# Performance work log

Measured on AMD Instinct MI355X. Metric: run time of the kernel, lower is better.

The kernel has to match this reference:

```python
import jax, jax.numpy as jnp
import numpy as np

NNZ = 4_194_304
IN_FEATURES = 4096
OUT_FEATURES = 4096
BATCH = 4
SEQ = 2048


def setup_inputs() -> dict:
    key = jax.random.key(0)
    k1, k2, k3, k4, k5, k6 = jax.random.split(key, 6)
    x = jax.random.normal(k1, (BATCH, SEQ, IN_FEATURES), dtype=jnp.float32)
    rows = jax.random.randint(k2, (NNZ,), 0, OUT_FEATURES, dtype=jnp.int32)
    cols = jax.random.randint(k3, (NNZ,), 0, IN_FEATURES, dtype=jnp.int32)
    w_real = jax.random.normal(k4, (NNZ,), dtype=jnp.float32)
    w_imag = jax.random.normal(k5, (NNZ,), dtype=jnp.float32)
    phase_angles = jax.random.uniform(k6, (BATCH,), dtype=jnp.float32) * 2.0 * np.pi
    return {
        "x": x,
        "rows": rows,
        "cols": cols,
        "w_real": w_real,
        "w_imag": w_imag,
        "phase_angles": phase_angles,
        "out_features": OUT_FEATURES,
    }


def reference(x, rows, cols, w_real, w_imag, phase_angles, out_features):
    B, S, F_in = x.shape
    N = B * S
    x_flat = x.reshape(N, F_in)  # [N, F_in]
    # per-flattened-row cosine phase (phase is per-batch, repeated over seq)
    cos_p = jnp.cos(jnp.repeat(phase_angles, S))  # [N]
    # assemble sparse COO weights into dense (out, in) matrices (duplicates sum)
    Wr = jnp.zeros((out_features, F_in), dtype=x_flat.dtype).at[rows, cols].add(w_real)
    Wi = jnp.zeros((out_features, F_in), dtype=x_flat.dtype).at[rows, cols].add(w_imag)
    # out[n, r] = sum_e x[n, cols[e]] * (w_real[e] + cos(phase[n]) * w_imag[e])
    out = x_flat @ Wr.T + cos_p[:, None] * (x_flat @ Wi.T)  # [N, out]
    return out.reshape(B, S, out_features)
```

## Files before the change

kernel.cpp:

```cpp
#include <hip/hip_runtime.h>


#define K_IN   4096
#define F_OUT  4096
#define SEQ    2048
#define NROW   8192
#define NNZ    4194304
#define WELEM  16777216
#define NBUCK  1024
#define SEGB   5120

typedef float  f32x4  __attribute__((ext_vector_type(4)));
typedef __bf16 bf16x8 __attribute__((ext_vector_type(8)));
typedef unsigned short u16x8 __attribute__((ext_vector_type(8)));

__device__ __forceinline__ unsigned short f2bf(float f) {
  unsigned u = __builtin_bit_cast(unsigned, f);
  u += 0x7fffu + ((u >> 16) & 1u);
  return (unsigned short)(u >> 16);
}
__device__ __forceinline__ float bf2f(unsigned short b) {
  return __builtin_bit_cast(float, (unsigned)b << 16);
}

__global__ __launch_bounds__(1024) void bin_kernel(
    const int* __restrict__ rows, const int* __restrict__ cols,
    const float* __restrict__ wre, const float* __restrict__ wim,
    unsigned* __restrict__ cursor, unsigned long long* __restrict__ records,
    const float* __restrict__ x, unsigned short* __restrict__ Xb) {
  const int b = blockIdx.x;
  if (b < 256) {
    __shared__ unsigned cnt[NBUCK];
    const int tid = threadIdx.x;
    const int e0 = b << 14;
    cnt[tid] = 0u;
    __syncthreads();
    #pragma unroll
    for (int i = 0; i < 16; ++i)
      atomicAdd(&cnt[((unsigned)rows[e0 + (i << 10) + tid]) >> 2], 1u);
    __syncthreads();
    {
      const unsigned c = cnt[tid];
      unsigned base = 0u;
      if (c) base = atomicAdd(&cursor[tid], c);
      cnt[tid] = base;
    }
    __syncthreads();
    for (int i = 0; i < 16; ++i) {
      const int e = e0 + (i << 10) + tid;
      const unsigned r  = (unsigned)rows[e];
      const unsigned bk = r >> 2;
      const unsigned rank = atomicAdd(&cnt[bk], 1u);
      const unsigned pk = (unsigned)f2bf(wre[e]) | ((unsigned)f2bf(wim[e]) << 16);
      if (rank < SEGB)
        records[(size_t)bk * SEGB + rank] =
            ((unsigned long long)pk << 32) | ((r & 3u) << 12) | (unsigned)cols[e];
    }
  } else {
    const size_t i8 = (((size_t)(b - 256) << 10) + threadIdx.x) << 3;
    f32x4 a = *(const f32x4*)(x + i8);
    f32x4 c = *(const f32x4*)(x + i8 + 4);
    u16x8 v;
    v[0] = f2bf(a[0]); v[1] = f2bf(a[1]); v[2] = f2bf(a[2]); v[3] = f2bf(a[3]);
    v[4] = f2bf(c[0]); v[5] = f2bf(c[1]); v[6] = f2bf(c[2]); v[7] = f2bf(c[3]);
    *(u16x8*)(Xb + i8) = v;
  }
}

__global__ __launch_bounds__(1024) void assemble_kernel(
    const unsigned* __restrict__ cursor,
    const unsigned long long* __restrict__ records,
    const float* __restrict__ phase, unsigned short* __restrict__ Wb) {
  __shared__ float accRe[16384];
  __shared__ float accIm[16384];
  const int bk  = blockIdx.x;
  const int tid = threadIdx.x;
  #pragma unroll
  for (int i = 0; i < 16; ++i) {
    accRe[(i << 10) + tid] = 0.f;
    accIm[(i << 10) + tid] = 0.f;
  }
  __syncthreads();
  unsigned cnt = cursor[bk];
  if (cnt > SEGB) cnt = SEGB;
  const unsigned long long* seg = records + (size_t)bk * SEGB;
  for (unsigned i = tid; i < cnt; i += 1024) {
    const unsigned long long rec = seg[i];
    const unsigned s = (unsigned)rec & 16383u;
    atomicAdd(&accRe[s], bf2f((unsigned short)((rec >> 32) & 0xffffu)));
    atomicAdd(&accIm[s], bf2f((unsigned short)(rec >> 48)));
  }
  __syncthreads();
  float cb[4];
  cb[0] = cosf(phase[0]); cb[1] = cosf(phase[1]);
  cb[2] = cosf(phase[2]); cb[3] = cosf(phase[3]);
  #pragma unroll
  for (int it = 0; it < 16; ++it) {
    const int s = (it << 10) + tid;
    const float re = accRe[s];
    const float im = accIm[s];
    #pragma unroll
    for (int bb = 0; bb < 4; ++bb)
      Wb[((size_t)bb << 24) + ((size_t)bk << 14) + s] = f2bf(re + cb[bb] * im);
  }
}

#define GLOAD_LDS(g, l)                                                        \
  __builtin_amdgcn_global_load_lds(                                            \
      (const __attribute__((address_space(1))) unsigned int*)(g),              \
      (__attribute__((address_space(3))) unsigned int*)(l), 16, 0, 0)

__global__ __launch_bounds__(512, 2) void gemm_kernel(
    const unsigned short* __restrict__ Xb,
    const unsigned short* __restrict__ Wb,
    float* __restrict__ out) {
  __shared__ unsigned short lds[65536];

  const int tid  = threadIdx.x;
  const int wid  = tid >> 6;
  const int lane = tid & 63;
  const int wr   = wid >> 2;
  const int wc   = wid & 3;

  const int bid  = blockIdx.x;
  const int swz  = ((bid & 7) << 6) | (bid >> 3);
  const int brow = swz >> 4;
  const int bcol = swz & 15;
  const size_t M0 = (size_t)brow << 8;
  const int batch = brow >> 3;
  const unsigned short* Ap = Xb + M0 * K_IN;
  const unsigned short* Bp = Wb + ((size_t)batch << 24) + (((size_t)bcol << 8) * K_IN);

  const int srow = lane >> 3;
  const int gsl  = ((lane & 7) ^ srow) << 3;
  const int lrow = lane & 15;
  const int lr7  = lane & 7;
  const int sb   = lane >> 4;

  f32x4 acc[8][4] = {};

#define STAGE(buf, k0)                                                         \
  {                                                                            \
    _Pragma("unroll")                                                          \
    for (int l = 0; l < 4; ++l) {                                              \
      const int rr = (l << 6) + (wid << 3);                                    \
      GLOAD_LDS(Ap + (size_t)(rr + srow) * K_IN + (size_t)((k0) + gsl),        \
                &lds[((buf) << 15) + (rr << 6)]);                              \
    }                                                                          \
    _Pragma("unroll")                                                          \
    for (int l = 0; l < 4; ++l) {                                              \
      const int rr = (l << 6) + (wid << 3);                                    \
      GLOAD_LDS(Bp + (size_t)(rr + srow) * K_IN + (size_t)((k0) + gsl),        \
                &lds[((buf) << 15) + 16384 + (rr << 6)]);                      \
    }                                                                          \
  }

#define COMPUTE(buf)                                                           \
  {                                                                            \
    const unsigned short* la = &lds[(buf) << 15];                              \
    const unsigned short* lb = &lds[((buf) << 15) + 16384];                    \
    _Pragma("unroll")                                                          \
    for (int t = 0; t < 2; ++t) {                                              \
      const int cs = (((t << 2) + sb) ^ lr7) << 3;                             \
      bf16x8 af[8], bff[4];                                                    \
      _Pragma("unroll")                                                        \
      for (int m = 0; m < 8; ++m)                                              \
        af[m] = *(const bf16x8*)&la[(((wr << 7) + (m << 4) + lrow) << 6) + cs];\
      _Pragma("unroll")                                                        \
      for (int n = 0; n < 4; ++n)                                              \
        bff[n] = *(const bf16x8*)&lb[(((wc << 6) + (n << 4) + lrow) << 6) + cs];\
      __builtin_amdgcn_s_setprio(1);                                           \
      _Pragma("unroll")                                                        \
      for (int m = 0; m < 8; ++m)                                              \
        _Pragma("unroll")                                                      \
        for (int n = 0; n < 4; ++n)                                            \
          acc[m][n] = __builtin_amdgcn_mfma_f32_16x16x32_bf16(                 \
              af[m], bff[n], acc[m][n], 0, 0, 0);                              \
      __builtin_amdgcn_s_setprio(0);                                           \
    }                                                                          \
  }

  STAGE(0, 0);
  int cur = 0;
  for (int t = 0; t < 63; ++t) {
    STAGE(cur ^ 1, (t + 1) << 6);
    asm volatile("s_waitcnt vmcnt(8)\n\ts_barrier" ::: "memory");
    COMPUTE(cur);
    asm volatile("s_waitcnt lgkmcnt(0)\n\ts_barrier" ::: "memory");
    cur ^= 1;
  }
  asm volatile("s_waitcnt vmcnt(0)\n\ts_barrier" ::: "memory");
  COMPUTE(cur);

  const int ch = lane >> 4;
  float* op = out + (M0 + (size_t)(wr << 7)) * F_OUT + ((size_t)bcol << 8) + (wc << 6);
  #pragma unroll
  for (int m = 0; m < 8; ++m)
    #pragma unroll
    for (int n = 0; n < 4; ++n)
      #pragma unroll
      for (int j = 0; j < 4; ++j)
        op[(size_t)((m << 4) + (ch << 2) + j) * F_OUT + (n << 4) + lrow] = acc[m][n][j];
#undef STAGE
#undef COMPUTE
}

__global__ __launch_bounds__(256) void scatter_kernel(
    const int* __restrict__ rows, const int* __restrict__ cols,
    const float* __restrict__ wre, const float* __restrict__ wim,
    unsigned short* __restrict__ Wcb) {
  int e = blockIdx.x * 256 + threadIdx.x;
  int r = rows[e];
  int c = cols[e];
  unsigned pk = (unsigned)f2bf(wre[e]) | ((unsigned)f2bf(wim[e]) << 16);
  size_t idx = ((size_t)r << 12) + (size_t)c;
  asm volatile("global_atomic_pk_add_bf16 %0, %1, off"
               :: "v"(Wcb + (idx << 1)), "v"(pk) : "memory");
}
__global__ __launch_bounds__(256) void fold_kernel(
    const unsigned short* __restrict__ Wcb, const float* __restrict__ phase,
    unsigned short* __restrict__ Wb) {
  size_t i8 = ((size_t)blockIdx.x * 256 + threadIdx.x) << 3;
  float cb[4];
  cb[0] = cosf(phase[0]); cb[1] = cosf(phase[1]);
  cb[2] = cosf(phase[2]); cb[3] = cosf(phase[3]);
  const unsigned short* p = Wcb + (i8 << 1);
  u16x8 a = *(const u16x8*)(p);
  u16x8 b = *(const u16x8*)(p + 8);
  float rr[8], ii[8];
  rr[0] = bf2f(a[0]); ii[0] = bf2f(a[1]);
  rr[1] = bf2f(a[2]); ii[1] = bf2f(a[3]);
  rr[2] = bf2f(a[4]); ii[2] = bf2f(a[5]);
  rr[3] = bf2f(a[6]); ii[3] = bf2f(a[7]);
  rr[4] = bf2f(b[0]); ii[4] = bf2f(b[1]);
  rr[5] = bf2f(b[2]); ii[5] = bf2f(b[3]);
  rr[6] = bf2f(b[4]); ii[6] = bf2f(b[5]);
  rr[7] = bf2f(b[6]); ii[7] = bf2f(b[7]);
  #pragma unroll
  for (int bb = 0; bb < 4; ++bb) {
    float c = cb[bb];
    u16x8 v;
    #pragma unroll
    for (int j = 0; j < 8; ++j) v[j] = f2bf(rr[j] + c * ii[j]);
    *(u16x8*)(Wb + ((size_t)bb << 24) + i8) = v;
  }
}
__global__ __launch_bounds__(256) void xconv_kernel(
    const float* __restrict__ x, unsigned short* __restrict__ Xb) {
  size_t i8 = ((size_t)blockIdx.x * 256 + threadIdx.x) << 3;
  f32x4 a = *(const f32x4*)(x + i8);
  f32x4 c = *(const f32x4*)(x + i8 + 4);
  u16x8 v;
  v[0] = f2bf(a[0]); v[1] = f2bf(a[1]); v[2] = f2bf(a[2]); v[3] = f2bf(a[3]);
  v[4] = f2bf(c[0]); v[5] = f2bf(c[1]); v[6] = f2bf(c[2]); v[7] = f2bf(c[3]);
  *(u16x8*)(Xb + i8) = v;
}
__global__ __launch_bounds__(256) void naive_kernel(
    const float* __restrict__ x, const unsigned short* __restrict__ Wcb,
    const float* __restrict__ phase, float* __restrict__ out) {
  int n = blockIdx.x >> 4;
  int r = ((blockIdx.x & 15) << 8) | threadIdx.x;
  float cb = cosf(phase[n >> 11]);
  const float* xp = x + ((size_t)n << 12);
  const unsigned short* wc = Wcb + (((size_t)r << 12) << 1);
  float ar = 0.f, ai = 0.f;
  for (int k = 0; k < K_IN; ++k) {
    float xv = xp[k];
    ar += xv * bf2f(wc[2 * k]);
    ai += xv * bf2f(wc[2 * k + 1]);
  }
  out[((size_t)n << 12) + r] = ar + cb * ai;
}

extern "C" void kernel_launch(void* const* d_in, const int* in_sizes, int n_in,
                              void* d_out, int out_size, void* d_ws, size_t ws_size,
                              hipStream_t stream) {
  const float* x     = (const float*)d_in[0];
  const int*   rows  = (const int*)d_in[1];
  const int*   cols  = (const int*)d_in[2];
  const float* wre   = (const float*)d_in[3];
  const float* wim   = (const float*)d_in[4];
  const float* phase = (const float*)d_in[5];
  float* out = (float*)d_out;

  const size_t WS_FULL = (size_t)268435456;
  const size_t WS_MAIN = (size_t)201326592;
  if (ws_size >= WS_FULL) {
    unsigned short*     Wb      = (unsigned short*)d_ws;
    unsigned short*     Xb      = (unsigned short*)((char*)d_ws + (size_t)134217728);
    unsigned long long* records = (unsigned long long*)((char*)d_ws + (size_t)201326592);
    unsigned*           cursor  = (unsigned*)((char*)d_ws + (size_t)251658240);
    hipMemsetAsync(cursor, 0, NBUCK * sizeof(unsigned), stream);
    bin_kernel<<<256 + 4096, 1024, 0, stream>>>(rows, cols, wre, wim,
                                                cursor, records, x, Xb);
    assemble_kernel<<<NBUCK, 1024, 0, stream>>>(cursor, records, phase, Wb);
    gemm_kernel<<<512, 512, 0, stream>>>(Xb, Wb, out);
  } else if (ws_size >= WS_MAIN) {
    unsigned short* Wcb = (unsigned short*)d_ws;
    unsigned short* Wb  = (unsigned short*)((char*)d_ws + (size_t)67108864);
    unsigned short* Xb  = (unsigned short*)d_ws;
    hipMemsetAsync(d_ws, 0, (size_t)WELEM * 4, stream);
    scatter_kernel<<<NNZ / 256, 256, 0, stream>>>(rows, cols, wre, wim, Wcb);
    fold_kernel<<<WELEM / 8 / 256, 256, 0, stream>>>(Wcb, phase, Wb);
    xconv_kernel<<<(size_t)NROW * K_IN / 8 / 256, 256, 0, stream>>>(x, Xb);
    gemm_kernel<<<512, 512, 0, stream>>>(Xb, Wb, out);
  } else {
    unsigned short* Wcb = (unsigned short*)d_ws;
    hipMemsetAsync(d_ws, 0, (size_t)WELEM * 4, stream);
    scatter_kernel<<<NNZ / 256, 256, 0, stream>>>(rows, cols, wre, wim, Wcb);
    naive_kernel<<<NROW * 16, 256, 0, stream>>>(x, Wcb, phase, out);
  }
}
```

Before: 459.2 us.

## Switch GEMM mainloop to 4-stage LDS pipeline with K=32 tiles

The bf16 GEMM mainloop drops from a double-buffered K=64 tile to a four-buffer ring of K=32 tiles, so three tiles are in flight while one is computed. The LDS swizzle is redone for the 32-element row width, and the per-stage wait count is raised to keep more global-to-LDS loads outstanding. The goal is to hide global memory latency better. The cost is twice as many barriers per K and half the MFMA work per stage, so barrier overhead is larger relative to compute.

```diff
diff --git a/kernel.cpp b/kernel.cpp
--- a/kernel.cpp
+++ b/kernel.cpp
@@ -131,66 +131,73 @@
   const unsigned short* Ap = Xb + M0 * K_IN;
   const unsigned short* Bp = Wb + ((size_t)batch << 24) + (((size_t)bcol << 8) * K_IN);
 
-  const int srow = lane >> 3;
-  const int gsl  = ((lane & 7) ^ srow) << 3;
+  const int srow4 = lane >> 2;
+  const int gsl   = (((lane & 3) ^ ((lane >> 2) & 3) ^ ((lane >> 4) & 3)) << 3);
   const int lrow = lane & 15;
-  const int lr7  = lane & 7;
   const int sb   = lane >> 4;
+  const int fsl  = ((sb ^ (lrow & 3) ^ ((lrow >> 2) & 3)) << 3);
 
   f32x4 acc[8][4] = {};
 
-#define STAGE(buf, k0)                                                         \
+#define STAGE(buf, kt)                                                         \
   {                                                                            \
     _Pragma("unroll")                                                          \
-    for (int l = 0; l < 4; ++l) {                                              \
-      const int rr = (l << 6) + (wid << 3);                                    \
-      GLOAD_LDS(Ap + (size_t)(rr + srow) * K_IN + (size_t)((k0) + gsl),        \
-                &lds[((buf) << 15) + (rr << 6)]);                              \
+    for (int l = 0; l < 2; ++l) {                                              \
+      const int rb = (l << 7) + (wid << 4);                                    \
+      GLOAD_LDS(Ap + (size_t)(rb + srow4) * K_IN + (size_t)(((kt) << 5) + gsl),\
+                &lds[((buf) << 14) + (rb << 5)]);                              \
     }                                                                          \
     _Pragma("unroll")                                                          \
-    for (int l = 0; l < 4; ++l) {                                              \
-      const int rr = (l << 6) + (wid << 3);                                    \
-      GLOAD_LDS(Bp + (size_t)(rr + srow) * K_IN + (size_t)((k0) + gsl),        \
-                &lds[((buf) << 15) + 16384 + (rr << 6)]);                      \
+    for (int l = 0; l < 2; ++l) {                                              \
+      const int rb = (l << 7) + (wid << 4);                                    \
+      GLOAD_LDS(Bp + (size_t)(rb + srow4) * K_IN + (size_t)(((kt) << 5) + gsl),\
+                &lds[((buf) << 14) + 8192 + (rb << 5)]);                       \
     }                                                                          \
   }
 
 #define COMPUTE(buf)                                                           \
   {                                                                            \
-    const unsigned short* la = &lds[(buf) << 15];                              \
-    const unsigned short* lb = &lds[((buf) << 15) + 16384];                    \
-    _Pragma("unroll")                                                          \
-    for (int t = 0; t < 2; ++t) {                                              \
-      const int cs = (((t << 2) + sb) ^ lr7) << 3;                             \
-      bf16x8 af[8], bff[4];                                                    \
-      _Pragma("unroll")                                                        \
-      for (int m = 0; m < 8; ++m)                                              \
-        af[m] = *(const bf16x8*)&la[(((wr << 7) + (m << 4) + lrow) << 6) + cs];\
+    const unsigned short* la = &lds[(buf) << 14];                              \
+    const unsigned short* lb = la + 8192;                                      \
+    bf16x8 af[8], bff[4];                                                      \
+    _Pragma("unroll")                                                          \
+    for (int m = 0; m < 8; ++m)                                                \
+      af[m] = *(const bf16x8*)&la[(((wr << 7) + (m << 4) + lrow) << 5) + fsl]; \
+    _Pragma("unroll")                                                          \
+    for (int n = 0; n < 4; ++n)                                                \
+      bff[n] = *(const bf16x8*)&lb[(((wc << 6) + (n << 4) + lrow) << 5) + fsl];\
+    __builtin_amdgcn_s_setprio(1);                                             \
+    _Pragma("unroll")                                                          \
+    for (int m = 0; m < 8; ++m)                                                \
       _Pragma("unroll")                                                        \
       for (int n = 0; n < 4; ++n)                                              \
-        bff[n] = *(const bf16x8*)&lb[(((wc << 6) + (n << 4) + lrow) << 6) + cs];\
-      __builtin_amdgcn_s_setprio(1);                                           \
-      _Pragma("unroll")                                                        \
-      for (int m = 0; m < 8; ++m)                                              \
-        _Pragma("unroll")                                                      \
-        for (int n = 0; n < 4; ++n)                                            \
-          acc[m][n] = __builtin_amdgcn_mfma_f32_16x16x32_bf16(                 \
-              af[m], bff[n], acc[m][n], 0, 0, 0);                              \
-      __builtin_amdgcn_s_setprio(0);                                           \
-    }                                                                          \
-  }
-
-  STAGE(0, 0);
-  int cur = 0;
-  for (int t = 0; t < 63; ++t) {
-    STAGE(cur ^ 1, (t + 1) << 6);
-    asm volatile("s_waitcnt vmcnt(8)\n\ts_barrier" ::: "memory");
-    COMPUTE(cur);
-    asm volatile("s_waitcnt lgkmcnt(0)\n\ts_barrier" ::: "memory");
-    cur ^= 1;
-  }
+        acc[m][n] = __builtin_amdgcn_mfma_f32_16x16x32_bf16(                   \
+            af[m], bff[n], acc[m][n], 0, 0, 0);                                \
+    __builtin_amdgcn_s_setprio(0);                                             \
+  }
+
+#define STEP(cb, sbuf, kt)                                                     \
+  {                                                                            \
+    STAGE(sbuf, kt);                                                           \
+    asm volatile("s_waitcnt vmcnt(12)\n\ts_barrier" ::: "memory");             \
+    COMPUTE(cb);                                                               \
+    asm volatile("s_waitcnt lgkmcnt(0)\n\ts_barrier" ::: "memory");            \
+  }
+
+  STAGE(0, 0); STAGE(1, 1); STAGE(2, 2);
+  for (int I = 0; I < 31; ++I) {
+    const int t = I << 2;
+    STEP(0, 3, t + 3); STEP(1, 0, t + 4); STEP(2, 1, t + 5); STEP(3, 2, t + 6);
+  }
+  STEP(0, 3, 127);
+  asm volatile("s_waitcnt vmcnt(8)\n\ts_barrier" ::: "memory");
+  COMPUTE(1);
+  asm volatile("s_waitcnt lgkmcnt(0)\n\ts_barrier" ::: "memory");
+  asm volatile("s_waitcnt vmcnt(4)\n\ts_barrier" ::: "memory");
+  COMPUTE(2);
+  asm volatile("s_waitcnt lgkmcnt(0)\n\ts_barrier" ::: "memory");
   asm volatile("s_waitcnt vmcnt(0)\n\ts_barrier" ::: "memory");
-  COMPUTE(cur);
+  COMPUTE(3);
 
   const int ch = lane >> 4;
   float* op = out + (M0 + (size_t)(wr << 7)) * F_OUT + ((size_t)bcol << 8) + (wc << 6);
@@ -203,6 +210,7 @@
         op[(size_t)((m << 4) + (ch << 2) + j) * F_OUT + (n << 4) + lrow] = acc[m][n][j];
 #undef STAGE
 #undef COMPUTE
+#undef STEP
 }
 
 __global__ __launch_bounds__(256) void scatter_kernel(
```

After: 446.6 us. 1.03x faster.
